# Kernel tuning notes

Measured on AMD Instinct MI355X. Metric: run time of the kernel, lower is better.

## Reference

```python
import jax, jax.numpy as jnp
import numpy as np

K, S, P = 3, 2, 2  # kernel_size, stride, padding (dilation=1)


def _unfold(xp, k, s, oh, ow):
    """Extract k*k strided patches from a padded array.

    xp: (..., Hp, Wp) -> (..., k*k, oh, ow), window-position ordering (kh, kw)
    matching torch.nn.Unfold (channel-major handled by caller).
    """
    return jnp.stack(
        [xp[..., i:i + s * (oh - 1) + 1:s, j:j + s * (ow - 1) + 1:s]
         for i in range(K) for j in range(K)],
        axis=-3,
    )


def setup_inputs() -> dict:
    key = jax.random.key(0)
    x = jax.random.normal(key, (8, 256, 128, 128), dtype=jnp.float32)
    return {"x": x}


def reference(x):
    b, c, h, w = x.shape
    oh = (h - K + 2 * P) // S + 1
    ow = (w - K + 2 * P) // S + 1

    # channel-wise L2 norm, computed BEFORE unfolding (padding contributes 0 either way)
    n = jnp.sqrt(jnp.sum(x * x, axis=1))            # (b, h, w)
    n_pad = jnp.pad(n, ((0, 0), (P, P), (P, P)))
    n_patch = _unfold(n_pad, K, S, oh, ow)          # (b, k*k, oh, ow)
    # weighting_fn = softmax over the k*k window positions (torch dim=1 of unfolded norm)
    wts = jax.nn.softmax(n_patch, axis=1)           # (b, k*k, oh, ow)

    x_pad = jnp.pad(x, ((0, 0), (0, 0), (P, P), (P, P)))
    x_patch = _unfold(x_pad, K, S, oh, ow)          # (b, c, k*k, oh, ow)

    # weighted sum over window positions
    return jnp.sum(wts[:, None] * x_patch, axis=2)  # (b, c, oh, ow)
```

## Files before the change

### kernel.cpp

```cpp
#include <hip/hip_runtime.h>
#include <math.h>

#define BATCH 8
#define CH    256
#define H     128
#define W     128
#define HW    (H * W)
#define OH    65
#define OW    65
#define NPIX  (OH * OW)
#define TPB   512
#define WAVES 8
#define CPW   (CH / WAVES)
#define TASKS (CPW * OW)
#define ITERS ((TASKS + 63) / 64)

__global__ __launch_bounds__(TPB) void fused_kernel(const float* __restrict__ x,
                                                    float* __restrict__ out) {
    const int bx   = blockIdx.x;
    const int b    = bx / OH;
    const int oh   = bx - b * OH;
    const int tid  = threadIdx.x;
    const int lane = tid & 63;
    const int wv   = tid >> 6;

    int  rowc[3];
    bool rv[3];
    #pragma unroll
    for (int r = 0; r < 3; ++r) {
        int ih = oh * 2 + r - 2;
        rv[r]   = (unsigned)ih < (unsigned)H;
        rowc[r] = ih < 0 ? 0 : (ih > H - 1 ? H - 1 : ih);
    }

    __shared__ float part[WAVES][3][W];
    __shared__ float nrm[3][W];
    __shared__ float wls[OH][11];

    const float* xw = x + (size_t)(b * CH + wv * CPW) * HW;
    float2 a0 = {0.f, 0.f}, a1 = {0.f, 0.f}, a2 = {0.f, 0.f};
    #pragma unroll 4
    for (int c = 0; c < CPW; ++c) {
        const float* xp = xw + (size_t)c * HW;
        float2 v0 = *(const float2*)(xp + rowc[0] * W + 2 * lane);
        float2 v1 = *(const float2*)(xp + rowc[1] * W + 2 * lane);
        float2 v2 = *(const float2*)(xp + rowc[2] * W + 2 * lane);
        a0.x += v0.x * v0.x; a0.y += v0.y * v0.y;
        a1.x += v1.x * v1.x; a1.y += v1.y * v1.y;
        a2.x += v2.x * v2.x; a2.y += v2.y * v2.y;
    }
    *(float2*)&part[wv][0][2 * lane] = a0;
    *(float2*)&part[wv][1][2 * lane] = a1;
    *(float2*)&part[wv][2][2 * lane] = a2;
    __syncthreads();

    if (tid < 3 * W) {
        int r = tid >> 7, col = tid & (W - 1);
        float s = 0.f;
        #pragma unroll
        for (int w = 0; w < WAVES; ++w) s += part[w][r][col];
        nrm[r][col] = sqrtf(s);
    }
    __syncthreads();

    if (tid < OH) {
        const int ow  = tid;
        const int iw0 = ow * 2 - 2;
        float nv[9];
        bool  val[9];
        float m = 0.0f;
        #pragma unroll
        for (int kh = 0; kh < 3; ++kh) {
            bool vh = rv[kh];
            #pragma unroll
            for (int kw = 0; kw < 3; ++kw) {
                int iw = iw0 + kw;
                int k  = kh * 3 + kw;
                bool v = vh && ((unsigned)iw < (unsigned)W);
                val[k] = v;
                nv[k]  = v ? nrm[kh][iw] : 0.0f;
                m = fmaxf(m, nv[k]);
            }
        }
        float denom = 0.0f, wt[9];
        #pragma unroll
        for (int k = 0; k < 9; ++k) {
            float e = __expf(nv[k] - m);
            denom += e;
            wt[k] = val[k] ? e : 0.0f;
        }
        float inv = 1.0f / denom;
        #pragma unroll
        for (int k = 0; k < 9; ++k) wls[ow][k] = wt[k] * inv;
    }
    __syncthreads();

    float* ob = out + (size_t)(b * CH + wv * CPW) * NPIX + (size_t)oh * OW;
    #pragma unroll 2
    for (int it = 0; it < ITERS; ++it) {
        int id = it * 64 + lane;
        if (id < TASKS) {
            int c  = id / OW;
            int ow = id - c * OW;
            int iw0 = ow * 2 - 2;
            int iwa = iw0 < 0 ? 0 : iw0;
            int iwc = (iw0 + 2) > (W - 1) ? (W - 1) : (iw0 + 2);
            float w0 = wls[ow][0], w1 = wls[ow][1], w2 = wls[ow][2];
            float w3 = wls[ow][3], w4 = wls[ow][4], w5 = wls[ow][5];
            float w6 = wls[ow][6], w7 = wls[ow][7], w8 = wls[ow][8];
            const float* xc = xw + (size_t)c * HW;
            const float* r0 = xc + rowc[0] * W;
            const float* r1 = xc + rowc[1] * W;
            const float* r2 = xc + rowc[2] * W;
            float2 p0 = *(const float2*)(r0 + iwa);
            float2 p1 = *(const float2*)(r1 + iwa);
            float2 p2 = *(const float2*)(r2 + iwa);
            float  s0 = r0[iwc], s1 = r1[iwc], s2 = r2[iwc];
            float acc = w0 * p0.x + w1 * p0.y + w2 * s0
                      + w3 * p1.x + w4 * p1.y + w5 * s1
                      + w6 * p2.x + w7 * p2.y + w8 * s2;
            ob[(size_t)c * NPIX + ow] = acc;
        }
    }
}

extern "C" void kernel_launch(void* const* d_in, const int* in_sizes, int n_in,
                              void* d_out, int out_size, void* d_ws, size_t ws_size,
                              hipStream_t stream) {
    const float* x = (const float*)d_in[0];
    float* out = (float*)d_out;
    (void)d_ws; (void)ws_size;
    fused_kernel<<<BATCH * OH, TPB, 0, stream>>>(x, out);
}
```

Measured before the change: 251.8 us.

## Keep input rows in registers and compute outputs via lane shuffles

Each thread now loads its three input rows for all 32 of its channels into registers once. Those registers serve both the channel-norm reduction and the weighted 3x3 sum, so x is no longer reloaded from global memory in a second pass. The output is split into a per-lane partial, which is passed to the neighbouring lane with __shfl_up, replacing per-task divides and gathers. Block indexing is also reordered so batch varies fastest. The cost is about 192 VGPRs per thread for the cached values, which may lower occupancy or cause spills.

New measurement: 215.3 us. 1.17x faster.

```diff
diff --git a/kernel.cpp b/kernel.cpp
--- a/kernel.cpp
+++ b/kernel.cpp
@@ -12,14 +12,11 @@
 #define TPB   512
 #define WAVES 8
 #define CPW   (CH / WAVES)
-#define TASKS (CPW * OW)
-#define ITERS ((TASKS + 63) / 64)
 
 __global__ __launch_bounds__(TPB) void fused_kernel(const float* __restrict__ x,
                                                     float* __restrict__ out) {
-    const int bx   = blockIdx.x;
-    const int b    = bx / OH;
-    const int oh   = bx - b * OH;
+    const int b    = blockIdx.x & 7;
+    const int oh   = blockIdx.x >> 3;
     const int tid  = threadIdx.x;
     const int lane = tid & 63;
     const int wv   = tid >> 6;
@@ -35,19 +32,27 @@
 
     __shared__ float part[WAVES][3][W];
     __shared__ float nrm[3][W];
-    __shared__ float wls[OH][11];
+    __shared__ float wls[OH][9];
 
-    const float* xw = x + (size_t)(b * CH + wv * CPW) * HW;
+    const float2* xw2 = (const float2*)x + (size_t)(b * CH + wv * CPW) * (HW / 2);
+    const int base0 = rowc[0] * (W / 2) + lane;
+    const int base1 = rowc[1] * (W / 2) + lane;
+    const int base2 = rowc[2] * (W / 2) + lane;
+
+    float2 xv[CPW][3];
     float2 a0 = {0.f, 0.f}, a1 = {0.f, 0.f}, a2 = {0.f, 0.f};
-    #pragma unroll 4
+    #pragma unroll
     for (int c = 0; c < CPW; ++c) {
-        const float* xp = xw + (size_t)c * HW;
-        float2 v0 = *(const float2*)(xp + rowc[0] * W + 2 * lane);
-        float2 v1 = *(const float2*)(xp + rowc[1] * W + 2 * lane);
-        float2 v2 = *(const float2*)(xp + rowc[2] * W + 2 * lane);
-        a0.x += v0.x * v0.x; a0.y += v0.y * v0.y;
-        a1.x += v1.x * v1.x; a1.y += v1.y * v1.y;
-        a2.x += v2.x * v2.x; a2.y += v2.y * v2.y;
+        const size_t cb = (size_t)c * (HW / 2);
+        xv[c][0] = xw2[cb + base0];
+        xv[c][1] = xw2[cb + base1];
+        xv[c][2] = xw2[cb + base2];
+    }
+    #pragma unroll
+    for (int c = 0; c < CPW; ++c) {
+        a0.x += xv[c][0].x * xv[c][0].x; a0.y += xv[c][0].y * xv[c][0].y;
+        a1.x += xv[c][1].x * xv[c][1].x; a1.y += xv[c][1].y * xv[c][1].y;
+        a2.x += xv[c][2].x * xv[c][2].x; a2.y += xv[c][2].y * xv[c][2].y;
     }
     *(float2*)&part[wv][0][2 * lane] = a0;
     *(float2*)&part[wv][1][2 * lane] = a1;
@@ -95,32 +100,25 @@
     }
     __syncthreads();
 
+    const float wA0 = wls[lane][2], wA1 = wls[lane][5], wA2 = wls[lane][8];
+    const float wB0 = wls[lane + 1][0], wC0 = wls[lane + 1][1];
+    const float wB1 = wls[lane + 1][3], wC1 = wls[lane + 1][4];
+    const float wB2 = wls[lane + 1][6], wC2 = wls[lane + 1][7];
+
     float* ob = out + (size_t)(b * CH + wv * CPW) * NPIX + (size_t)oh * OW;
-    #pragma unroll 2
-    for (int it = 0; it < ITERS; ++it) {
-        int id = it * 64 + lane;
-        if (id < TASKS) {
-            int c  = id / OW;
-            int ow = id - c * OW;
-            int iw0 = ow * 2 - 2;
-            int iwa = iw0 < 0 ? 0 : iw0;
-            int iwc = (iw0 + 2) > (W - 1) ? (W - 1) : (iw0 + 2);
-            float w0 = wls[ow][0], w1 = wls[ow][1], w2 = wls[ow][2];
-            float w3 = wls[ow][3], w4 = wls[ow][4], w5 = wls[ow][5];
-            float w6 = wls[ow][6], w7 = wls[ow][7], w8 = wls[ow][8];
-            const float* xc = xw + (size_t)c * HW;
-            const float* r0 = xc + rowc[0] * W;
-            const float* r1 = xc + rowc[1] * W;
-            const float* r2 = xc + rowc[2] * W;
-            float2 p0 = *(const float2*)(r0 + iwa);
-            float2 p1 = *(const float2*)(r1 + iwa);
-            float2 p2 = *(const float2*)(r2 + iwa);
-            float  s0 = r0[iwc], s1 = r1[iwc], s2 = r2[iwc];
-            float acc = w0 * p0.x + w1 * p0.y + w2 * s0
-                      + w3 * p1.x + w4 * p1.y + w5 * s1
-                      + w6 * p2.x + w7 * p2.y + w8 * s2;
-            ob[(size_t)c * NPIX + ow] = acc;
-        }
+    #pragma unroll
+    for (int c = 0; c < CPW; ++c) {
+        const float vx0 = xv[c][0].x, vy0 = xv[c][0].y;
+        const float vx1 = xv[c][1].x, vy1 = xv[c][1].y;
+        const float vx2 = xv[c][2].x, vy2 = xv[c][2].y;
+        float S = wB0 * vx0 + wC0 * vy0
+                + wB1 * vx1 + wC1 * vy1
+                + wB2 * vx2 + wC2 * vy2;
+        float T = wA0 * vx0 + wA1 * vx1 + wA2 * vx2;
+        float Sp = __shfl_up(S, 1);
+        float res = (lane == 0) ? T : T + Sp;
+        ob[(size_t)c * NPIX + lane] = res;
+        if (lane == 63) ob[(size_t)c * NPIX + 64] = S;
     }
 }
 
```
